# Performance work log

Measured on AMD Instinct MI355X. Metric: run time of the kernel, lower is better.

The kernel has to match this reference:

```python
import jax, jax.numpy as jnp
import numpy as np

N = 256      # N' = N (pair rep crop size)
CZ = 128     # c_z
H = 4        # num_heads
DH = 32      # c_hidden per head
INF = 1e9
EPS = 1e-5

def setup_inputs() -> dict:
    key = jax.random.key(0)
    ks = jax.random.split(key, 8)
    s = 0.02
    return {
        "x": jax.random.normal(ks[0], (N, N, CZ), jnp.float32),
        "mask": jnp.ones((N, N), jnp.float32),
        "ln_g": jnp.ones((CZ,), jnp.float32),
        "ln_b": jnp.zeros((CZ,), jnp.float32),
        "w_tri": jax.random.normal(ks[1], (H, CZ), jnp.float32) * s,   # Linear(c_z -> H), no bias
        "wq": jax.random.normal(ks[2], (H * DH, CZ), jnp.float32) * s,
        "wk": jax.random.normal(ks[3], (H * DH, CZ), jnp.float32) * s,
        "wv": jax.random.normal(ks[4], (H * DH, CZ), jnp.float32) * s,
        "wg": jax.random.normal(ks[5], (H * DH, CZ), jnp.float32) * s,
        "bg": jnp.ones((H * DH,), jnp.float32),   # gating bias init = 1 (OpenFold)
        "wo": jax.random.normal(ks[6], (CZ, H * DH), jnp.float32) * s,
        "bo": jnp.zeros((CZ,), jnp.float32),
    }

def reference(x, mask, ln_g, ln_b, w_tri, wq, wk, wv, wg, bg, wo, bo):
    # starting=True -> no transpose. LayerNorm over c_z.
    mu = jnp.mean(x, axis=-1, keepdims=True)
    var = jnp.var(x, axis=-1, keepdims=True)
    xn = (x - mu) * jax.lax.rsqrt(var + EPS) * ln_g + ln_b        # [N', N, CZ]

    # mask bias: [*, N', 1, 1, N]
    mask_bias = (INF * (mask - 1.0))[..., :, None, None, :]
    # triangle bias: linear -> [N', N, H] -> permute (2,0,1) -> [H, N', N] -> [1, H, N', N]
    tri_bias = jnp.einsum('...ijc,hc->...hij', xn, w_tri)[..., None, :, :, :]

    scale = 1.0 / np.sqrt(DH).astype(np.float32)
    wq3, wk3, wv3, wg3 = (w.reshape(H, DH, CZ) for w in (wq, wk, wv, wg))
    q = jnp.einsum('...qc,hdc->...qhd', xn, wq3) * scale           # [N', N, H, DH]
    k = jnp.einsum('...kc,hdc->...khd', xn, wk3)
    v = jnp.einsum('...kc,hdc->...khd', xn, wv3)

    logits = jnp.einsum('...qhd,...khd->...hqk', q, k) + mask_bias + tri_bias  # [N', H, N, N]
    a = jax.nn.softmax(logits, axis=-1)
    o = jnp.einsum('...hqk,...khd->...qhd', a, v)                  # [N', N, H, DH]

    g = jax.nn.sigmoid(jnp.einsum('...qc,hdc->...qhd', xn, wg3) + bg.reshape(H, DH))
    o = (o * g).reshape(*o.shape[:-2], H * DH)                     # [N', N, H*DH]
    return jnp.einsum('...qe,oe->...qo', o, wo) + bo               # [N', N, CZ]
```

## Files before the change

kernel.cpp:

```cpp
#include <hip/hip_runtime.h>
#include <hip/hip_bf16.h>
#include <math.h>


#define NN 256
#define CZ 128
#define NH 4
#define DH 32
#define NPOS (NN * NN)
#define PSZ ((size_t)NPOS * CZ)
#define SCALE 0.17677669529663687f

typedef unsigned short ushort_t;
using f32x4  = __attribute__((ext_vector_type(4))) float;
using bf16x8 = __attribute__((ext_vector_type(8))) short;
using bf16x4 = __attribute__((ext_vector_type(4))) short;

__device__ __forceinline__ float sigmoidf_(float x) {
    return 1.0f / (1.0f + __expf(-x));
}
__device__ __forceinline__ ushort_t f2bf(float f) {
    unsigned u = __float_as_uint(f);
    u = (u + 0x7fffu + ((u >> 16) & 1u)) >> 16;
    return (ushort_t)u;
}
__device__ __forceinline__ float bf2f(ushort_t b) {
    return __uint_as_float(((unsigned)b) << 16);
}
__device__ __forceinline__ float trunc_bf(float f) {
    return __uint_as_float(__float_as_uint(f) & 0xffff0000u);
}
__device__ __forceinline__ bf16x4 pack_bf4(float a, float b, float c, float d) {
    union { unsigned u[2]; bf16x4 v; } r;
    r.u[0] = (__float_as_uint(b) & 0xffff0000u) | (__float_as_uint(a) >> 16);
    r.u[1] = (__float_as_uint(d) & 0xffff0000u) | (__float_as_uint(c) >> 16);
    return r.v;
}
__device__ __forceinline__ bf16x4 pack_bf4_rne(float a, float b, float c, float d) {
    union { ushort_t s[4]; bf16x4 v; } r;
    r.s[0] = f2bf(a); r.s[1] = f2bf(b); r.s[2] = f2bf(c); r.s[3] = f2bf(d);
    return r.v;
}

#define SX(row, lc) ((row) * 64 + ((((lc) ^ ((row) & 7))) << 3))

__global__ __launch_bounds__(256)
void convert_weights(const float* __restrict__ wq, const float* __restrict__ wk,
                     const float* __restrict__ wv, const float* __restrict__ wg,
                     const float* __restrict__ wo,
                     ushort_t* __restrict__ Wc_hi, ushort_t* __restrict__ Wc_lo,
                     ushort_t* __restrict__ wo_hi, ushort_t* __restrict__ wo_lo) {
    int idx = blockIdx.x * 256 + threadIdx.x;
    float x;
    if (idx < 65536) {
        int t = idx >> 14;
        const float* src = (t == 0) ? wq : (t == 1) ? wk : (t == 2) ? wv : wg;
        x = src[idx & 16383];
        ushort_t h = f2bf(x);
        Wc_hi[idx] = h;
        Wc_lo[idx] = f2bf(x - bf2f(h));
    } else {
        int r = idx - 65536;
        x = wo[r];
        ushort_t h = f2bf(x);
        wo_hi[r] = h;
        wo_lo[r] = f2bf(x - bf2f(h));
    }
}

__global__ __launch_bounds__(256)
void ln_qkvg_kernel(const float* __restrict__ x,
                    const float* __restrict__ ln_g,
                    const float* __restrict__ ln_b,
                    const float* __restrict__ w_tri,
                    const ushort_t* __restrict__ Wc_hi,
                    const ushort_t* __restrict__ Wc_lo,
                    float* __restrict__ tri,
                    ushort_t* __restrict__ qbo, ushort_t* __restrict__ kbo,
                    ushort_t* __restrict__ vto, float* __restrict__ gfo) {
    __shared__ ushort_t sXh[2][64 * 64];
    __shared__ ushort_t sXl[2][64 * 64];

    const int tid = threadIdx.x;
    const int p0 = blockIdx.x * 64;
    const int g16 = tid >> 4;
    const int cg  = tid & 15;

    float4 gv0 = *(const float4*)(ln_g + cg * 8);
    float4 gv1 = *(const float4*)(ln_g + cg * 8 + 4);
    float4 bv0 = *(const float4*)(ln_b + cg * 8);
    float4 bv1 = *(const float4*)(ln_b + cg * 8 + 4);
    float wtf[4][8];
    #pragma unroll
    for (int h = 0; h < 4; h++) {
        float4 w0 = *(const float4*)(w_tri + h * CZ + cg * 8);
        float4 w1 = *(const float4*)(w_tri + h * CZ + cg * 8 + 4);
        wtf[h][0] = w0.x; wtf[h][1] = w0.y; wtf[h][2] = w0.z; wtf[h][3] = w0.w;
        wtf[h][4] = w1.x; wtf[h][5] = w1.y; wtf[h][6] = w1.z; wtf[h][7] = w1.w;
    }
    float gg[8] = {gv0.x, gv0.y, gv0.z, gv0.w, gv1.x, gv1.y, gv1.z, gv1.w};
    float bb[8] = {bv0.x, bv0.y, bv0.z, bv0.w, bv1.x, bv1.y, bv1.z, bv1.w};

    #pragma unroll
    for (int pp = 0; pp < 4; pp++) {
        int row = pp * 16 + g16;
        const float* xp = x + (size_t)(p0 + row) * CZ + cg * 8;
        float4 a = *(const float4*)xp;
        float4 b = *(const float4*)(xp + 4);
        float xv[8] = {a.x, a.y, a.z, a.w, b.x, b.y, b.z, b.w};
        float s = 0.f, sq = 0.f;
        #pragma unroll
        for (int e = 0; e < 8; e++) { s += xv[e]; sq += xv[e] * xv[e]; }
        #pragma unroll
        for (int off = 1; off < 16; off <<= 1) {
            s  += __shfl_xor(s,  off);
            sq += __shfl_xor(sq, off);
        }
        float mu = s * (1.0f / 128.0f);
        float var = sq * (1.0f / 128.0f) - mu * mu;
        float rs = rsqrtf(var + 1e-5f);

        float xn[8];
        float t0 = 0.f, t1 = 0.f, t2 = 0.f, t3 = 0.f;
        union { ushort_t sv[8]; uint4 u; } H, L;
        #pragma unroll
        for (int e = 0; e < 8; e++) {
            xn[e] = (xv[e] - mu) * rs * gg[e] + bb[e];
            H.sv[e] = f2bf(xn[e]);
            L.sv[e] = f2bf(xn[e] - bf2f(H.sv[e]));
            t0 += xn[e] * wtf[0][e];
            t1 += xn[e] * wtf[1][e];
            t2 += xn[e] * wtf[2][e];
            t3 += xn[e] * wtf[3][e];
        }
        *(uint4*)&sXh[cg >> 3][SX(row, cg & 7)] = H.u;
        *(uint4*)&sXl[cg >> 3][SX(row, cg & 7)] = L.u;

        #pragma unroll
        for (int off = 1; off < 16; off <<= 1) {
            t0 += __shfl_xor(t0, off);
            t1 += __shfl_xor(t1, off);
            t2 += __shfl_xor(t2, off);
            t3 += __shfl_xor(t3, off);
        }
        if (cg == 0) {
            int p = p0 + row;
            int i = p >> 8, j = p & 255;
            int kt = j >> 6, mt = (j >> 4) & 3, kg2 = (j >> 2) & 3, r = j & 3;
            int wv2 = i >> 6, nt = (i >> 4) & 3, lr2 = i & 15;
            size_t base = ((((size_t)(kt * 16 + mt * 4 + wv2)) * 4 + nt) * 64 +
                           kg2 * 16 + lr2) * 4 + r;
            tri[base + 0 * 65536] = t0;
            tri[base + 1 * 65536] = t1;
            tri[base + 2 * 65536] = t2;
            tri[base + 3 * 65536] = t3;
        }
    }
    __syncthreads();

    const int lane = tid & 63;
    const int t = tid >> 6;
    const int lr = lane & 15, kg = lane >> 4;
    const int i_ = p0 >> 8;
    const int j0 = p0 & 255;

    const ushort_t* whb = Wc_hi + ((size_t)(t * 128 + lr)) * CZ + kg * 8;
    const ushort_t* wlb = Wc_lo + ((size_t)(t * 128 + lr)) * CZ + kg * 8;

    #pragma unroll
    for (int np = 0; np < 2; np++) {
        f32x4 acc[4][4];
        #pragma unroll
        for (int a = 0; a < 4; a++)
            #pragma unroll
            for (int b = 0; b < 4; b++) acc[a][b] = (f32x4){0.f, 0.f, 0.f, 0.f};

        #pragma unroll
        for (int ks = 0; ks < 4; ks++) {
            bf16x8 xh[4], xl[4];
            #pragma unroll
            for (int mt = 0; mt < 4; mt++) {
                xh[mt] = *(bf16x8*)&sXh[ks >> 1][SX(mt * 16 + lr, (ks & 1) * 4 + kg)];
                xl[mt] = *(bf16x8*)&sXl[ks >> 1][SX(mt * 16 + lr, (ks & 1) * 4 + kg)];
            }
            #pragma unroll
            for (int nt = 0; nt < 4; nt++) {
                int n = np * 64 + nt * 16;
                bf16x8 wh = *(const bf16x8*)(whb + (size_t)n * CZ + ks * 32);
                bf16x8 wl = *(const bf16x8*)(wlb + (size_t)n * CZ + ks * 32);
                if (t == 2) {
                    #pragma unroll
                    for (int mt = 0; mt < 4; mt++) {
                        acc[mt][nt] = __builtin_amdgcn_mfma_f32_16x16x32_bf16(xh[mt], wh, acc[mt][nt], 0, 0, 0);
                        acc[mt][nt] = __builtin_amdgcn_mfma_f32_16x16x32_bf16(xl[mt], wh, acc[mt][nt], 0, 0, 0);
                        acc[mt][nt] = __builtin_amdgcn_mfma_f32_16x16x32_bf16(xh[mt], wl, acc[mt][nt], 0, 0, 0);
                    }
                } else {
                    #pragma unroll
                    for (int mt = 0; mt < 4; mt++) {
                        acc[nt][mt] = __builtin_amdgcn_mfma_f32_16x16x32_bf16(wh, xh[mt], acc[nt][mt], 0, 0, 0);
                        acc[nt][mt] = __builtin_amdgcn_mfma_f32_16x16x32_bf16(wh, xl[mt], acc[nt][mt], 0, 0, 0);
                        acc[nt][mt] = __builtin_amdgcn_mfma_f32_16x16x32_bf16(wl, xh[mt], acc[nt][mt], 0, 0, 0);
                    }
                }
            }
        }

        if (t == 2) {
            #pragma unroll
            for (int mt = 0; mt < 4; mt++) {
                int j = j0 + mt * 16 + kg * 4;
                #pragma unroll
                for (int nt = 0; nt < 4; nt++) {
                    int c = np * 64 + nt * 16 + lr;
                    int h = c >> 5, d = c & 31;
                    size_t ihb = (size_t)((i_ << 2) + h) * 8192;
                    *(bf16x4*)(vto + ihb + (size_t)d * 256 + j) =
                        pack_bf4_rne(acc[mt][nt][0], acc[mt][nt][1],
                                     acc[mt][nt][2], acc[mt][nt][3]);
                }
            }
        } else {
            #pragma unroll
            for (int mt = 0; mt < 4; mt++) {
                int j = j0 + mt * 16 + lr;
                #pragma unroll
                for (int nt = 0; nt < 4; nt++) {
                    int c = np * 64 + nt * 16 + kg * 4;
                    int h = c >> 5, d = c & 31;
                    size_t base = (size_t)((i_ << 2) + h) * 8192 + (size_t)j * 32 + d;
                    if (t == 0) {
                        *(bf16x4*)(qbo + base) = pack_bf4_rne(
                            acc[nt][mt][0] * SCALE, acc[nt][mt][1] * SCALE,
                            acc[nt][mt][2] * SCALE, acc[nt][mt][3] * SCALE);
                    } else if (t == 1) {
                        *(bf16x4*)(kbo + base) = pack_bf4_rne(
                            acc[nt][mt][0], acc[nt][mt][1],
                            acc[nt][mt][2], acc[nt][mt][3]);
                    } else {
                        float4 o;
                        o.x = acc[nt][mt][0]; o.y = acc[nt][mt][1];
                        o.z = acc[nt][mt][2]; o.w = acc[nt][mt][3];
                        *(float4*)(gfo + base) = o;
                    }
                }
            }
        }
    }
}

__global__ __launch_bounds__(256)
void gemm_direct_kernel(const ushort_t* __restrict__ Xhi, const ushort_t* __restrict__ Xlo,
                        const ushort_t* __restrict__ Whi, const ushort_t* __restrict__ Wlo,
                        float* __restrict__ out0, const float* __restrict__ bias) {
    const int tid = threadIdx.x;
    const int bm = blockIdx.x;
    const int lane = tid & 63;
    const int wv_ = tid >> 6;
    const int wm = wv_ >> 1, wn = wv_ & 1;
    const int lr = lane & 15, kg = lane >> 4;

    const ushort_t* xh_base = Xhi + ((size_t)(bm * 128 + wm * 64 + lr)) * CZ + kg * 8;
    const ushort_t* xl_base = Xlo + ((size_t)(bm * 128 + wm * 64 + lr)) * CZ + kg * 8;
    const ushort_t* wh_base = Whi + ((size_t)(wn * 64 + lr)) * CZ + kg * 8;
    const ushort_t* wl_base = Wlo + ((size_t)(wn * 64 + lr)) * CZ + kg * 8;

    f32x4 acc[4][4];
    #pragma unroll
    for (int a = 0; a < 4; a++)
        #pragma unroll
        for (int b = 0; b < 4; b++) acc[a][b] = (f32x4){0.f, 0.f, 0.f, 0.f};

    #pragma unroll
    for (int ks = 0; ks < 4; ks++) {
        bf16x8 xh[4], xl[4], wh[4], wl[4];
        #pragma unroll
        for (int mt = 0; mt < 4; mt++) {
            xh[mt] = *(const bf16x8*)(xh_base + (size_t)mt * 16 * CZ + ks * 32);
            xl[mt] = *(const bf16x8*)(xl_base + (size_t)mt * 16 * CZ + ks * 32);
        }
        #pragma unroll
        for (int nt = 0; nt < 4; nt++) {
            wh[nt] = *(const bf16x8*)(wh_base + (size_t)nt * 16 * CZ + ks * 32);
            wl[nt] = *(const bf16x8*)(wl_base + (size_t)nt * 16 * CZ + ks * 32);
        }
        #pragma unroll
        for (int nt = 0; nt < 4; nt++)
            #pragma unroll
            for (int mt = 0; mt < 4; mt++) {
                acc[nt][mt] = __builtin_amdgcn_mfma_f32_16x16x32_bf16(wh[nt], xh[mt], acc[nt][mt], 0, 0, 0);
                acc[nt][mt] = __builtin_amdgcn_mfma_f32_16x16x32_bf16(wl[nt], xh[mt], acc[nt][mt], 0, 0, 0);
                acc[nt][mt] = __builtin_amdgcn_mfma_f32_16x16x32_bf16(wh[nt], xl[mt], acc[nt][mt], 0, 0, 0);
            }
    }

    #pragma unroll
    for (int mt = 0; mt < 4; mt++) {
        int m = bm * 128 + wm * 64 + mt * 16 + lr;
        #pragma unroll
        for (int nt = 0; nt < 4; nt++) {
            int nb = wn * 64 + nt * 16 + kg * 4;
            float4 bv = *(const float4*)(bias + nb);
            float4 o;
            o.x = acc[nt][mt][0] + bv.x;
            o.y = acc[nt][mt][1] + bv.y;
            o.z = acc[nt][mt][2] + bv.z;
            o.w = acc[nt][mt][3] + bv.w;
            *(float4*)(out0 + (size_t)m * CZ + nb) = o;
        }
    }
}

__global__ __launch_bounds__(256, 4)
void attn_mfma_kernel(const ushort_t* __restrict__ qb,
                      const ushort_t* __restrict__ kb,
                      const ushort_t* __restrict__ vtb,
                      const float* __restrict__ gf,
                      const float* __restrict__ tri,
                      const float* __restrict__ mask,
                      const float* __restrict__ bg,
                      ushort_t* __restrict__ og_hi,
                      ushort_t* __restrict__ og_lo) {
    __shared__ ushort_t sV[32 * 264];

    const int bid = blockIdx.x;
    const int h = bid >> 8;
    const int i = bid & 255;
    const int tid = threadIdx.x;
    const int lane = tid & 63;
    const int wv_ = tid >> 6;
    const int lr = lane & 15;
    const int kg = lane >> 4;
    const int q0 = wv_ * 64;

    const size_t ih = (size_t)((i << 2) + h);
    const ushort_t* qp = qb + ih * 8192;
    const ushort_t* kp = kb + ih * 8192;
    const ushort_t* vp = vtb + ih * 8192;
    const float* mrow = mask + (i << 8);

    #pragma unroll
    for (int w = 0; w < 4; w++) {
        int idx = tid + w * 256;
        int d = idx >> 5, c = idx & 31;
        *(uint4*)&sV[d * 264 + c * 8] = *(const uint4*)(vp + d * 256 + c * 8);
    }

    bf16x8 qf[4];
    #pragma unroll
    for (int nt = 0; nt < 4; nt++)
        qf[nt] = *(const bf16x8*)(qp + (size_t)(q0 + nt * 16 + lr) * 32 + kg * 8);

    float tl[4] = {0.f, 0.f, 0.f, 0.f};
    f32x4 o[4][2];
    #pragma unroll
    for (int nt = 0; nt < 4; nt++) {
        o[nt][0] = (f32x4){0.f, 0.f, 0.f, 0.f};
        o[nt][1] = (f32x4){0.f, 0.f, 0.f, 0.f};
    }
    __syncthreads();

    #pragma unroll
    for (int kt = 0; kt < 4; kt++) {
        const int kt0 = kt * 64;
        #pragma unroll
        for (int mt = 0; mt < 4; mt++) {
            bf16x8 ka = *(const bf16x8*)(kp + (size_t)(kt0 + mt * 16 + lr) * 32 + kg * 8);
            const float* trib = tri + ((size_t)h << 16) +
                                ((((size_t)(kt * 16 + mt * 4 + wv_)) * 4) * 64 +
                                 kg * 16 + lr) * 4;
            float4 trif[4];
            #pragma unroll
            for (int nt = 0; nt < 4; nt++)
                trif[nt] = *(const float4*)(trib + (size_t)nt * 256);
            float4 mq = *(const float4*)(mrow + kt0 + mt * 16 + kg * 4);
            float mb[4] = {(mq.x - 1.f) * 1e9f, (mq.y - 1.f) * 1e9f,
                           (mq.z - 1.f) * 1e9f, (mq.w - 1.f) * 1e9f};

            f32x4 st[4];
            #pragma unroll
            for (int nt = 0; nt < 4; nt++)
                st[nt] = __builtin_amdgcn_mfma_f32_16x16x32_bf16(
                    ka, qf[nt], (f32x4){0.f, 0.f, 0.f, 0.f}, 0, 0, 0);

            bf16x4 pa[4];
            #pragma unroll
            for (int nt = 0; nt < 4; nt++) {
                float p0 = trunc_bf(__expf(st[nt][0] + mb[0] + trif[nt].x));
                float p1 = trunc_bf(__expf(st[nt][1] + mb[1] + trif[nt].y));
                float p2 = trunc_bf(__expf(st[nt][2] + mb[2] + trif[nt].z));
                float p3 = trunc_bf(__expf(st[nt][3] + mb[3] + trif[nt].w));
                tl[nt] += (p0 + p1) + (p2 + p3);
                pa[nt] = pack_bf4(p0, p1, p2, p3);
            }
            #pragma unroll
            for (int dt = 0; dt < 2; dt++) {
                bf16x4 vb = *(const bf16x4*)&sV[(dt * 16 + lr) * 264 + kt0 + mt * 16 + kg * 4];
                #pragma unroll
                for (int nt = 0; nt < 4; nt++)
                    o[nt][dt] = __builtin_amdgcn_mfma_f32_16x16x16bf16_1k(pa[nt], vb, o[nt][dt], 0, 0, 0);
            }
        }
    }

    #pragma unroll
    for (int nt = 0; nt < 4; nt++) {
        float t = tl[nt];
        t += __shfl_xor(t, 16);
        t += __shfl_xor(t, 32);
        float inv = 1.0f / t;
        #pragma unroll
        for (int r = 0; r < 4; r++) {
            float iv = __shfl(inv, kg * 4 + r, 16);
            int q = q0 + nt * 16 + kg * 4 + r;
            #pragma unroll
            for (int dt = 0; dt < 2; dt++) {
                int d = dt * 16 + lr;
                float gate = sigmoidf_(gf[ih * 8192 + q * 32 + d] + bg[(h << 5) + d]);
                float val = o[nt][dt][r] * iv * gate;
                ushort_t vh = f2bf(val);
                ushort_t vl = f2bf(val - bf2f(vh));
                size_t ofs = (size_t)((i << 8) + q) * CZ + (h << 5) + d;
                og_hi[ofs] = vh;
                og_lo[ofs] = vl;
            }
        }
    }
}

extern "C" void kernel_launch(void* const* d_in, const int* in_sizes, int n_in,
                              void* d_out, int out_size, void* d_ws, size_t ws_size,
                              hipStream_t stream) {
    const float* x     = (const float*)d_in[0];
    const float* mask  = (const float*)d_in[1];
    const float* ln_g  = (const float*)d_in[2];
    const float* ln_b  = (const float*)d_in[3];
    const float* w_tri = (const float*)d_in[4];
    const float* wq    = (const float*)d_in[5];
    const float* wk    = (const float*)d_in[6];
    const float* wv    = (const float*)d_in[7];
    const float* wg    = (const float*)d_in[8];
    const float* bg    = (const float*)d_in[9];
    const float* wo    = (const float*)d_in[10];
    const float* bo    = (const float*)d_in[11];
    float* out = (float*)d_out;

    float* ws = (float*)d_ws;
    float* tri = ws;
    float* gf  = ws + 262144;
    ushort_t* og_hi = (ushort_t*)(gf + PSZ);
    ushort_t* og_lo = og_hi + PSZ;
    ushort_t* qbuf  = og_lo + PSZ;
    ushort_t* kbuf  = qbuf + PSZ;
    ushort_t* vtbuf = kbuf + PSZ;
    ushort_t* Wc_hi = vtbuf + PSZ;
    ushort_t* Wc_lo = Wc_hi + 65536;
    ushort_t* wo_hi = Wc_lo + 65536;
    ushort_t* wo_lo = wo_hi + 16384;

    convert_weights<<<320, 256, 0, stream>>>(wq, wk, wv, wg, wo, Wc_hi, Wc_lo, wo_hi, wo_lo);
    ln_qkvg_kernel<<<NPOS / 64, 256, 0, stream>>>(
        x, ln_g, ln_b, w_tri, Wc_hi, Wc_lo, tri, qbuf, kbuf, vtbuf, gf);
    attn_mfma_kernel<<<NN * NH, 256, 0, stream>>>(
        qbuf, kbuf, vtbuf, gf, tri, mask, bg, og_hi, og_lo);
    gemm_direct_kernel<<<NPOS / 128, 256, 0, stream>>>(
        og_hi, og_lo, wo_hi, wo_lo, out, bo);
}
```

Before: 231.7 us.

## Fuse output projection into attention kernel and store gate pre-activation as fp16

The attention kernel is remapped so each block covers one row i and 64 queries across all four heads, one wave per head. The gated output is staged in shared memory as bf16 hi/lo and multiplied by Wo in the same kernel, so the separate output-projection GEMM and the og_hi/og_lo round trip through global memory go away. The gate pre-activation is now written and read as fp16 instead of fp32, halving that buffer's traffic. V is read straight from global instead of staged in LDS, and the fp16 gate rounding adds a little error.

```diff
diff --git a/kernel.cpp b/kernel.cpp
--- a/kernel.cpp
+++ b/kernel.cpp
@@ -29,6 +29,13 @@
 }
 __device__ __forceinline__ float trunc_bf(float f) {
     return __uint_as_float(__float_as_uint(f) & 0xffff0000u);
+}
+__device__ __forceinline__ ushort_t f2h(float f) {
+    _Float16 h = (_Float16)f;
+    union { _Float16 h; ushort_t u; } c; c.h = h; return c.u;
+}
+__device__ __forceinline__ float h2f(ushort_t u) {
+    union { ushort_t u; _Float16 h; } c; c.u = u; return (float)c.h;
 }
 __device__ __forceinline__ bf16x4 pack_bf4(float a, float b, float c, float d) {
     union { unsigned u[2]; bf16x4 v; } r;
@@ -77,7 +84,7 @@
                     const ushort_t* __restrict__ Wc_lo,
                     float* __restrict__ tri,
                     ushort_t* __restrict__ qbo, ushort_t* __restrict__ kbo,
-                    ushort_t* __restrict__ vto, float* __restrict__ gfo) {
+                    ushort_t* __restrict__ vto, ushort_t* __restrict__ gho) {
     __shared__ ushort_t sXh[2][64 * 64];
     __shared__ ushort_t sXl[2][64 * 64];
 
@@ -238,10 +245,12 @@
                             acc[nt][mt][0], acc[nt][mt][1],
                             acc[nt][mt][2], acc[nt][mt][3]);
                     } else {
-                        float4 o;
-                        o.x = acc[nt][mt][0]; o.y = acc[nt][mt][1];
-                        o.z = acc[nt][mt][2]; o.w = acc[nt][mt][3];
-                        *(float4*)(gfo + base) = o;
+                        ushort4 hv;
+                        hv.x = f2h(acc[nt][mt][0]);
+                        hv.y = f2h(acc[nt][mt][1]);
+                        hv.z = f2h(acc[nt][mt][2]);
+                        hv.w = f2h(acc[nt][mt][3]);
+                        *(ushort4*)(gho + base) = hv;
                     }
                 }
             }
@@ -249,89 +258,30 @@
     }
 }
 
-__global__ __launch_bounds__(256)
-void gemm_direct_kernel(const ushort_t* __restrict__ Xhi, const ushort_t* __restrict__ Xlo,
-                        const ushort_t* __restrict__ Whi, const ushort_t* __restrict__ Wlo,
-                        float* __restrict__ out0, const float* __restrict__ bias) {
-    const int tid = threadIdx.x;
-    const int bm = blockIdx.x;
-    const int lane = tid & 63;
-    const int wv_ = tid >> 6;
-    const int wm = wv_ >> 1, wn = wv_ & 1;
-    const int lr = lane & 15, kg = lane >> 4;
-
-    const ushort_t* xh_base = Xhi + ((size_t)(bm * 128 + wm * 64 + lr)) * CZ + kg * 8;
-    const ushort_t* xl_base = Xlo + ((size_t)(bm * 128 + wm * 64 + lr)) * CZ + kg * 8;
-    const ushort_t* wh_base = Whi + ((size_t)(wn * 64 + lr)) * CZ + kg * 8;
-    const ushort_t* wl_base = Wlo + ((size_t)(wn * 64 + lr)) * CZ + kg * 8;
-
-    f32x4 acc[4][4];
-    #pragma unroll
-    for (int a = 0; a < 4; a++)
-        #pragma unroll
-        for (int b = 0; b < 4; b++) acc[a][b] = (f32x4){0.f, 0.f, 0.f, 0.f};
-
-    #pragma unroll
-    for (int ks = 0; ks < 4; ks++) {
-        bf16x8 xh[4], xl[4], wh[4], wl[4];
-        #pragma unroll
-        for (int mt = 0; mt < 4; mt++) {
-            xh[mt] = *(const bf16x8*)(xh_base + (size_t)mt * 16 * CZ + ks * 32);
-            xl[mt] = *(const bf16x8*)(xl_base + (size_t)mt * 16 * CZ + ks * 32);
-        }
-        #pragma unroll
-        for (int nt = 0; nt < 4; nt++) {
-            wh[nt] = *(const bf16x8*)(wh_base + (size_t)nt * 16 * CZ + ks * 32);
-            wl[nt] = *(const bf16x8*)(wl_base + (size_t)nt * 16 * CZ + ks * 32);
-        }
-        #pragma unroll
-        for (int nt = 0; nt < 4; nt++)
-            #pragma unroll
-            for (int mt = 0; mt < 4; mt++) {
-                acc[nt][mt] = __builtin_amdgcn_mfma_f32_16x16x32_bf16(wh[nt], xh[mt], acc[nt][mt], 0, 0, 0);
-                acc[nt][mt] = __builtin_amdgcn_mfma_f32_16x16x32_bf16(wl[nt], xh[mt], acc[nt][mt], 0, 0, 0);
-                acc[nt][mt] = __builtin_amdgcn_mfma_f32_16x16x32_bf16(wh[nt], xl[mt], acc[nt][mt], 0, 0, 0);
-            }
-    }
-
-    #pragma unroll
-    for (int mt = 0; mt < 4; mt++) {
-        int m = bm * 128 + wm * 64 + mt * 16 + lr;
-        #pragma unroll
-        for (int nt = 0; nt < 4; nt++) {
-            int nb = wn * 64 + nt * 16 + kg * 4;
-            float4 bv = *(const float4*)(bias + nb);
-            float4 o;
-            o.x = acc[nt][mt][0] + bv.x;
-            o.y = acc[nt][mt][1] + bv.y;
-            o.z = acc[nt][mt][2] + bv.z;
-            o.w = acc[nt][mt][3] + bv.w;
-            *(float4*)(out0 + (size_t)m * CZ + nb) = o;
-        }
-    }
-}
-
 __global__ __launch_bounds__(256, 4)
-void attn_mfma_kernel(const ushort_t* __restrict__ qb,
-                      const ushort_t* __restrict__ kb,
-                      const ushort_t* __restrict__ vtb,
-                      const float* __restrict__ gf,
-                      const float* __restrict__ tri,
-                      const float* __restrict__ mask,
-                      const float* __restrict__ bg,
-                      ushort_t* __restrict__ og_hi,
-                      ushort_t* __restrict__ og_lo) {
-    __shared__ ushort_t sV[32 * 264];
+void attn_out_kernel(const ushort_t* __restrict__ qb,
+                     const ushort_t* __restrict__ kb,
+                     const ushort_t* __restrict__ vtb,
+                     const ushort_t* __restrict__ gh,
+                     const float* __restrict__ tri,
+                     const float* __restrict__ mask,
+                     const float* __restrict__ bg,
+                     const ushort_t* __restrict__ wo_hi,
+                     const ushort_t* __restrict__ wo_lo,
+                     const float* __restrict__ bo,
+                     float* __restrict__ out) {
+    __shared__ ushort_t sOgH[64 * 132];
+    __shared__ ushort_t sOgL[64 * 132];
 
     const int bid = blockIdx.x;
-    const int h = bid >> 8;
-    const int i = bid & 255;
+    const int i = bid >> 2;
+    const int qc = bid & 3;
     const int tid = threadIdx.x;
     const int lane = tid & 63;
-    const int wv_ = tid >> 6;
+    const int h = tid >> 6;
     const int lr = lane & 15;
     const int kg = lane >> 4;
-    const int q0 = wv_ * 64;
+    const int q0 = qc * 64;
 
     const size_t ih = (size_t)((i << 2) + h);
     const ushort_t* qp = qb + ih * 8192;
@@ -339,13 +289,6 @@
     const ushort_t* vp = vtb + ih * 8192;
     const float* mrow = mask + (i << 8);
 
-    #pragma unroll
-    for (int w = 0; w < 4; w++) {
-        int idx = tid + w * 256;
-        int d = idx >> 5, c = idx & 31;
-        *(uint4*)&sV[d * 264 + c * 8] = *(const uint4*)(vp + d * 256 + c * 8);
-    }
-
     bf16x8 qf[4];
     #pragma unroll
     for (int nt = 0; nt < 4; nt++)
@@ -358,7 +301,6 @@
         o[nt][0] = (f32x4){0.f, 0.f, 0.f, 0.f};
         o[nt][1] = (f32x4){0.f, 0.f, 0.f, 0.f};
     }
-    __syncthreads();
 
     #pragma unroll
     for (int kt = 0; kt < 4; kt++) {
@@ -367,7 +309,7 @@
         for (int mt = 0; mt < 4; mt++) {
             bf16x8 ka = *(const bf16x8*)(kp + (size_t)(kt0 + mt * 16 + lr) * 32 + kg * 8);
             const float* trib = tri + ((size_t)h << 16) +
-                                ((((size_t)(kt * 16 + mt * 4 + wv_)) * 4) * 64 +
+                                ((((size_t)(kt * 16 + mt * 4 + qc)) * 4) * 64 +
                                  kg * 16 + lr) * 4;
             float4 trif[4];
             #pragma unroll
@@ -395,7 +337,8 @@
             }
             #pragma unroll
             for (int dt = 0; dt < 2; dt++) {
-                bf16x4 vb = *(const bf16x4*)&sV[(dt * 16 + lr) * 264 + kt0 + mt * 16 + kg * 4];
+                bf16x4 vb = *(const bf16x4*)(vp + (size_t)(dt * 16 + lr) * 256 +
+                                             kt0 + mt * 16 + kg * 4);
                 #pragma unroll
                 for (int nt = 0; nt < 4; nt++)
                     o[nt][dt] = __builtin_amdgcn_mfma_f32_16x16x16bf16_1k(pa[nt], vb, o[nt][dt], 0, 0, 0);
@@ -403,6 +346,8 @@
         }
     }
 
+    float bgv0 = bg[(h << 5) + lr];
+    float bgv1 = bg[(h << 5) + 16 + lr];
     #pragma unroll
     for (int nt = 0; nt < 4; nt++) {
         float t = tl[nt];
@@ -412,18 +357,66 @@
         #pragma unroll
         for (int r = 0; r < 4; r++) {
             float iv = __shfl(inv, kg * 4 + r, 16);
-            int q = q0 + nt * 16 + kg * 4 + r;
+            int ql = nt * 16 + kg * 4 + r;
             #pragma unroll
             for (int dt = 0; dt < 2; dt++) {
                 int d = dt * 16 + lr;
-                float gate = sigmoidf_(gf[ih * 8192 + q * 32 + d] + bg[(h << 5) + d]);
+                float gate = sigmoidf_(h2f(gh[ih * 8192 + (size_t)(q0 + ql) * 32 + d]) +
+                                       (dt ? bgv1 : bgv0));
                 float val = o[nt][dt][r] * iv * gate;
                 ushort_t vh = f2bf(val);
-                ushort_t vl = f2bf(val - bf2f(vh));
-                size_t ofs = (size_t)((i << 8) + q) * CZ + (h << 5) + d;
-                og_hi[ofs] = vh;
-                og_lo[ofs] = vl;
-            }
+                int ofs = ql * 132 + (h << 5) + d;
+                sOgH[ofs] = vh;
+                sOgL[ofs] = f2bf(val - bf2f(vh));
+            }
+        }
+    }
+    __syncthreads();
+
+    const ushort_t* whb = wo_hi + (size_t)((h << 5) + lr) * CZ + kg * 8;
+    const ushort_t* wlb = wo_lo + (size_t)((h << 5) + lr) * CZ + kg * 8;
+
+    f32x4 acc[2][4];
+    #pragma unroll
+    for (int a = 0; a < 2; a++)
+        #pragma unroll
+        for (int b = 0; b < 4; b++) acc[a][b] = (f32x4){0.f, 0.f, 0.f, 0.f};
+
+    #pragma unroll
+    for (int ks = 0; ks < 4; ks++) {
+        bf16x8 ogh[4], ogl[4];
+        #pragma unroll
+        for (int mt = 0; mt < 4; mt++) {
+            int off = (mt * 16 + lr) * 132 + ks * 32 + kg * 8;
+            ogh[mt] = *(bf16x8*)&sOgH[off];
+            ogl[mt] = *(bf16x8*)&sOgL[off];
+        }
+        #pragma unroll
+        for (int nt = 0; nt < 2; nt++) {
+            bf16x8 wh = *(const bf16x8*)(whb + (size_t)(nt * 16) * CZ + ks * 32);
+            bf16x8 wl = *(const bf16x8*)(wlb + (size_t)(nt * 16) * CZ + ks * 32);
+            #pragma unroll
+            for (int mt = 0; mt < 4; mt++) {
+                acc[nt][mt] = __builtin_amdgcn_mfma_f32_16x16x32_bf16(wh, ogh[mt], acc[nt][mt], 0, 0, 0);
+                acc[nt][mt] = __builtin_amdgcn_mfma_f32_16x16x32_bf16(wl, ogh[mt], acc[nt][mt], 0, 0, 0);
+                acc[nt][mt] = __builtin_amdgcn_mfma_f32_16x16x32_bf16(wh, ogl[mt], acc[nt][mt], 0, 0, 0);
+            }
+        }
+    }
+
+    #pragma unroll
+    for (int mt = 0; mt < 4; mt++) {
+        int q = q0 + mt * 16 + lr;
+        #pragma unroll
+        for (int nt = 0; nt < 2; nt++) {
+            int n0 = (h << 5) + nt * 16 + kg * 4;
+            float4 bv = *(const float4*)(bo + n0);
+            float4 ov;
+            ov.x = acc[nt][mt][0] + bv.x;
+            ov.y = acc[nt][mt][1] + bv.y;
+            ov.z = acc[nt][mt][2] + bv.z;
+            ov.w = acc[nt][mt][3] + bv.w;
+            *(float4*)(out + (size_t)((i << 8) + q) * CZ + n0) = ov;
         }
     }
 }
@@ -447,10 +440,8 @@
 
     float* ws = (float*)d_ws;
     float* tri = ws;
-    float* gf  = ws + 262144;
-    ushort_t* og_hi = (ushort_t*)(gf + PSZ);
-    ushort_t* og_lo = og_hi + PSZ;
-    ushort_t* qbuf  = og_lo + PSZ;
+    ushort_t* ghbuf = (ushort_t*)(ws + 262144);
+    ushort_t* qbuf  = ghbuf + PSZ;
     ushort_t* kbuf  = qbuf + PSZ;
     ushort_t* vtbuf = kbuf + PSZ;
     ushort_t* Wc_hi = vtbuf + PSZ;
@@ -460,9 +451,7 @@
 
     convert_weights<<<320, 256, 0, stream>>>(wq, wk, wv, wg, wo, Wc_hi, Wc_lo, wo_hi, wo_lo);
     ln_qkvg_kernel<<<NPOS / 64, 256, 0, stream>>>(
-        x, ln_g, ln_b, w_tri, Wc_hi, Wc_lo, tri, qbuf, kbuf, vtbuf, gf);
-    attn_mfma_kernel<<<NN * NH, 256, 0, stream>>>(
-        qbuf, kbuf, vtbuf, gf, tri, mask, bg, og_hi, og_lo);
-    gemm_direct_kernel<<<NPOS / 128, 256, 0, stream>>>(
-        og_hi, og_lo, wo_hi, wo_lo, out, bo);
-}
+        x, ln_g, ln_b, w_tri, Wc_hi, Wc_lo, tri, qbuf, kbuf, vtbuf, ghbuf);
+    attn_out_kernel<<<NN * NH, 256, 0, stream>>>(
+        qbuf, kbuf, vtbuf, ghbuf, tri, mask, bg, wo_hi, wo_lo, bo, out);
+}
```

New measurement: 210.1 us. -9.3%, faster.
